# Optimization experiments

Hardware: AMD Instinct MI355X
Metric: run time of the kernel (lower is better)

## Reference

```python
import jax, jax.numpy as jnp
import numpy as np

GAMMA = 5.0 / 3.0
N, H = 131072, 256


def mlp(c, W1, b1, W2, b2, W3, b3, W4, b4):
    h = jnp.tanh(c @ W1 + b1)
    h = jnp.tanh(h @ W2 + b2)
    h = jnp.tanh(h @ W3 + b3)
    return h @ W4 + b4  # [N, 6] -> (rho, vx, vy, Bx, By, P)


def setup_inputs() -> dict:
    key = jax.random.key(0)
    ks = jax.random.split(key, 6)
    s = 0.5
    return {
        "coords": jax.random.uniform(ks[0], (N, 3), jnp.float32),  # (x, y, t)
        "W1": jax.random.normal(ks[1], (3, H), jnp.float32) * s,
        "b1": jnp.zeros((H,), jnp.float32),
        "W2": jax.random.normal(ks[2], (H, H), jnp.float32) * (s / np.sqrt(H)),
        "b2": jnp.zeros((H,), jnp.float32),
        "W3": jax.random.normal(ks[3], (H, H), jnp.float32) * (s / np.sqrt(H)),
        "b3": jnp.zeros((H,), jnp.float32),
        "W4": jax.random.normal(ks[4], (H, 6), jnp.float32) * (s / np.sqrt(H)),
        "b4": jnp.zeros((6,), jnp.float32),
        "weights": jnp.ones((7,), jnp.float32),
    }


def reference(coords, W1, b1, W2, b2, W3, b3, W4, b4, weights):
    f = lambda c: mlp(c, W1, b1, W2, b2, W3, b3, W4, b4)
    preds = f(coords)
    # Batched Jacobian d preds / d coords via 3 forward-mode JVPs (basis dirs x,y,t)
    eye = jnp.eye(3, dtype=coords.dtype)
    jvp1 = lambda e: jax.jvp(f, (coords,), (jnp.broadcast_to(e, coords.shape),))[1]
    J = jnp.transpose(jax.vmap(jvp1)(eye), (1, 2, 0))  # [N, 6, 3]

    rho, vx, vy, Bx, By, P = (preds[:, k] for k in range(6))
    Jx, Jy, Jt = J[..., 0], J[..., 1], J[..., 2]  # each [N, 6]

    # time derivatives (chain rule for composite fields)
    dt_rho = Jt[:, 0]
    dt_Bx, dt_By = Jt[:, 3], Jt[:, 4]
    dt_rhovx = dt_rho * vx + rho * Jt[:, 1]
    dt_rhovy = dt_rho * vy + rho * Jt[:, 2]

    def dE(Jc):  # derivative of total energy E along coord c
        return (Jc[:, 5] / (GAMMA - 1.0)
                + 0.5 * Jc[:, 0] * (vx ** 2 + vy ** 2)
                + rho * (vx * Jc[:, 1] + vy * Jc[:, 2])
                + Bx * Jc[:, 3] + By * Jc[:, 4])

    dE_dx, dE_dy, dE_dt = dE(Jx), dE(Jy), dE(Jt)

    div_v = Jx[:, 1] + Jy[:, 2]
    div_B = Jx[:, 3] + Jy[:, 4]
    continuity = dt_rho + rho * div_v

    # grad of total pressure P + 0.5*(Bx^2 + By^2)
    dPm_dx = Jx[:, 5] + Bx * Jx[:, 3] + By * Jx[:, 4]
    dPm_dy = Jy[:, 5] + Bx * Jy[:, 3] + By * Jy[:, 4]
    momentum_x = dt_rhovx + dPm_dx - (Bx * Jx[:, 3] + By * Jy[:, 3])
    momentum_y = dt_rhovy + dPm_dy - (Bx * Jx[:, 4] + By * Jy[:, 4])

    # induction: G = vx*By - vy*Bx
    def dG(Jc):
        return Jc[:, 1] * By + vx * Jc[:, 4] - Jc[:, 2] * Bx - vy * Jc[:, 3]

    induction_x = dt_Bx + dG(Jy)
    induction_y = dt_By - dG(Jx)

    # energy: d/dt E + div( S*v - D*B ), S = E + P + Pm, D = B.v
    E = P / (GAMMA - 1.0) + 0.5 * rho * (vx ** 2 + vy ** 2) + 0.5 * (Bx ** 2 + By ** 2)
    S = E + P + 0.5 * (Bx ** 2 + By ** 2)
    dS_dx = dE_dx + Jx[:, 5] + Bx * Jx[:, 3] + By * Jx[:, 4]
    dS_dy = dE_dy + Jy[:, 5] + Bx * Jy[:, 3] + By * Jy[:, 4]
    D = Bx * vx + By * vy

    def dD(Jc):
        return Jc[:, 3] * vx + Bx * Jc[:, 1] + Jc[:, 4] * vy + By * Jc[:, 2]

    dFx_dx = dS_dx * vx + S * Jx[:, 1] - dD(Jx) * Bx - D * Jx[:, 3]
    dFy_dy = dS_dy * vy + S * Jy[:, 2] - dD(Jy) * By - D * Jy[:, 4]
    energy = dE_dt + dFx_dx + dFy_dy

    res = [continuity, momentum_x, momentum_y, induction_x, induction_y, energy, div_B]
    loss = sum(w * jnp.mean(r ** 2) for w, r in zip(weights, res))
    return loss
```

## Files before the change

### kernel.cpp

```cpp
#include <hip/hip_runtime.h>
#include <hip/hip_bf16.h>
#include <cstdint>


#define LDW 264
#define TPTS 16
#define GRIDB 256

typedef __attribute__((ext_vector_type(8))) short v8h;
typedef __attribute__((ext_vector_type(4))) float v4f;

__device__ __forceinline__ ushort f2b(float f) {
    uint32_t u = __float_as_uint(f);
    u = (u + 0x7fffu + ((u >> 16) & 1u)) >> 16;
    return (ushort)u;
}
__device__ __forceinline__ uint32_t pk2(float a, float b) {
    union { __hip_bfloat162 h2; uint32_t u; } cv;
    cv.h2 = __float22bfloat162_rn(make_float2(a, b));
    return cv.u;
}
__device__ __forceinline__ float fast_tanh(float x) {
    float e = __expf(2.0f * x);
    return 1.0f - 2.0f * __builtin_amdgcn_rcpf(e + 1.0f);
}

__global__ void prep_weights(const float* __restrict__ W2, const float* __restrict__ W3,
                             const float* __restrict__ W4,
                             ushort* __restrict__ Wt2, ushort* __restrict__ Wt3,
                             ushort* __restrict__ Wt4) {
    int idx = blockIdx.x * 256 + threadIdx.x;
    if (idx < 65536) {
        int k = idx >> 8, n = idx & 255;
        Wt2[n * 256 + k] = f2b(W2[k * 256 + n]);
        Wt3[n * 256 + k] = f2b(W3[k * 256 + n]);
    }
    if (idx < 4096) {
        int n = idx >> 8, k = idx & 255;
        Wt4[n * 256 + k] = (n < 6) ? f2b(W4[k * 6 + n]) : (ushort)0;
    }
}

__device__ __forceinline__ void l1_point(ushort* __restrict__ Xd, const float* __restrict__ csb,
                                         int p, int jj0,
                                         float w0a, float w1a, float w2a, float ba,
                                         float w0b, float w1b, float w2b, float bb_) {
    float x = csb[p * 3], yc = csb[p * 3 + 1], tc = csb[p * 3 + 2];
    float pA = fmaf(x, w0a, fmaf(yc, w1a, fmaf(tc, w2a, ba)));
    float pB = fmaf(x, w0b, fmaf(yc, w1b, fmaf(tc, w2b, bb_)));
    float hA = fast_tanh(pA), hB = fast_tanh(pB);
    float dA = 1.0f - hA * hA, dB = 1.0f - hB * hB;
    *(uint32_t*)(&Xd[p * LDW + jj0])        = pk2(hA, hB);
    *(uint32_t*)(&Xd[(16 + p) * LDW + jj0]) = pk2(dA * w0a, dB * w0b);
    *(uint32_t*)(&Xd[(32 + p) * LDW + jj0]) = pk2(dA * w1a, dB * w1b);
    *(uint32_t*)(&Xd[(48 + p) * LDW + jj0]) = pk2(dA * w2a, dB * w2b);
}

__device__ __forceinline__ void dense_layer(const ushort* __restrict__ src,
                                            ushort* __restrict__ dst,
                                            const v8h (*wf)[8],
                                            const float* __restrict__ biasp,
                                            int wvg, int q, int l15) {
    v4f acc[4][4];
    #pragma unroll
    for (int a = 0; a < 4; a++)
        #pragma unroll
        for (int b = 0; b < 4; b++) {
            v4f z = {0.0f, 0.0f, 0.0f, 0.0f};
            acc[a][b] = z;
        }
    #pragma unroll
    for (int nt = 0; nt < 4; nt++) {
        const ushort* cb = &src[(nt * 16 + l15) * LDW + q * 8];
        v8h B[3];
        B[0] = *(const v8h*)(cb);
        B[1] = *(const v8h*)(cb + 32);
        #pragma unroll
        for (int kk = 0; kk < 8; kk++) {
            if (kk < 6)
                B[(kk + 2) % 3] = *(const v8h*)(cb + (kk + 2) * 32);
            const v8h Bc = B[kk % 3];
            #pragma unroll
            for (int mt = 0; mt < 4; mt++)
                acc[mt][nt] = __builtin_amdgcn_mfma_f32_16x16x32_bf16(
                                  wf[mt][kk], Bc, acc[mt][nt], 0, 0, 0);
        }
    }
    #pragma unroll
    for (int mt = 0; mt < 4; mt++) {
        const int nb = wvg * 64 + mt * 16 + q * 4;
        v4f bb = *(const v4f*)(&biasp[nb]);
        float h0 = fast_tanh(acc[mt][0][0] + bb[0]);
        float h1 = fast_tanh(acc[mt][0][1] + bb[1]);
        float h2 = fast_tanh(acc[mt][0][2] + bb[2]);
        float h3 = fast_tanh(acc[mt][0][3] + bb[3]);
        float d0 = 1.0f - h0 * h0, d1 = 1.0f - h1 * h1;
        float d2 = 1.0f - h2 * h2, d3 = 1.0f - h3 * h3;
        uint2 w;
        w.x = pk2(h0, h1); w.y = pk2(h2, h3);
        *(uint2*)(&dst[l15 * LDW + nb]) = w;
        #pragma unroll
        for (int s = 1; s < 4; s++) {
            w.x = pk2(d0 * acc[mt][s][0], d1 * acc[mt][s][1]);
            w.y = pk2(d2 * acc[mt][s][2], d3 * acc[mt][s][3]);
            *(uint2*)(&dst[(s * 16 + l15) * LDW + nb]) = w;
        }
    }
}

__global__ __launch_bounds__(512, 2)
void mhd_fused(const float* __restrict__ coords,
               const float* __restrict__ W1, const float* __restrict__ b1,
               const float* __restrict__ b2, const float* __restrict__ b3,
               const float* __restrict__ b4,
               const float* __restrict__ wts,
               const ushort* __restrict__ Wt2, const ushort* __restrict__ Wt3,
               const ushort* __restrict__ Wt4,
               float* __restrict__ out, int npts, float inv_n) {
    __shared__ ushort XsA[64 * LDW];
    __shared__ ushort XsB[2][64 * LDW];
    __shared__ ushort XsC[64 * LDW];
    __shared__ ushort W4s[16 * LDW];
    __shared__ float  bias_s[512];
    __shared__ float  cs[2][TPTS * 3];
    __shared__ float  Y4[2][4][TPTS][8];

    const int tid  = threadIdx.x;
    const int lane = tid & 63;
    const int wv   = tid >> 6;
    const int q    = lane >> 4;
    const int l15  = lane & 15;
    const int g3   = wv >> 2;
    const int wvg  = wv & 3;

    for (int idx = tid; idx < 16 * 256; idx += 512)
        W4s[(idx >> 8) * LDW + (idx & 255)] = Wt4[idx];
    bias_s[tid] = (tid < 256) ? b2[tid] : b3[tid - 256];

    const ushort* Wsrc = g3 ? Wt3 : Wt2;
    v8h wf[4][8];
    #pragma unroll
    for (int mt = 0; mt < 4; mt++) {
        const int nrow = (wvg * 64 + mt * 16 + l15) * 256 + q * 8;
        #pragma unroll
        for (int kk = 0; kk < 8; kk++)
            wf[mt][kk] = *(const v8h*)(&Wsrc[nrow + kk * 32]);
    }

    const int jj0 = (tid & 127) * 2, half8 = (tid >> 7) * 8;
    float w0a = 0, w1a = 0, w2a = 0, ba = 0, w0b = 0, w1b = 0, w2b = 0, bb_ = 0;
    if (!g3) {
        w0a = W1[jj0];       w1a = W1[256 + jj0];     w2a = W1[512 + jj0];     ba  = b1[jj0];
        w0b = W1[jj0 + 1];   w1b = W1[256 + jj0 + 1]; w2b = W1[512 + jj0 + 1]; bb_ = b1[jj0 + 1];
    }

    const float b40 = b4[0], b41 = b4[1], b42 = b4[2], b43 = b4[3], b44 = b4[4], b45 = b4[5];
    const float wt0 = wts[0], wt1 = wts[1], wt2_ = wts[2], wt3_ = wts[3],
                wt4_ = wts[4], wt5 = wts[5], wt6 = wts[6];

    const int ntiles = (npts + TPTS - 1) / TPTS;
    const int nt_blk = (ntiles > (int)blockIdx.x)
                         ? (ntiles - (int)blockIdx.x + GRIDB - 1) / GRIDB : 0;
    float vsum = 0.0f;

    if (tid < 96) {
        int b = tid / 48, r = tid % 48;
        if (b < nt_blk) {
            int p = r / 3, c = r % 3;
            int gp = ((int)blockIdx.x + b * GRIDB) * TPTS + p;
            if (gp >= npts) gp = npts - 1;
            cs[b][r] = coords[gp * 3 + c];
        }
    }
    __syncthreads();
    if (!g3 && nt_blk > 0) {
        #pragma unroll
        for (int pp = 0; pp < 8; pp++)
            l1_point(XsA, cs[0], half8 + pp, jj0, w0a, w1a, w2a, ba, w0b, w1b, w2b, bb_);
    }
    __syncthreads();

    for (int i = 0; i <= nt_blk + 1; ++i) {
        if (!g3) {
            if (i < nt_blk)
                dense_layer(XsA, XsB[i & 1], wf, bias_s, wvg, q, l15);
        } else {
            if (i >= 1 && i <= nt_blk)
                dense_layer(XsB[(i + 1) & 1], XsC, wf, bias_s + 256, wvg, q, l15);
        }
        __syncthreads();

        if (!g3) {
            if (i + 1 < nt_blk) {
                const float* csb = cs[(i + 1) & 1];
                #pragma unroll
                for (int pp = 0; pp < 8; pp++)
                    l1_point(XsA, csb, half8 + pp, jj0,
                             w0a, w1a, w2a, ba, w0b, w1b, w2b, bb_);
            }
        } else {
            if (i >= 1 && i <= nt_blk) {
                v4f a4 = {0.0f, 0.0f, 0.0f, 0.0f};
                #pragma unroll
                for (int kk = 0; kk < 8; kk++) {
                    v8h A  = *(const v8h*)(&W4s[l15 * LDW + kk * 32 + q * 8]);
                    v8h Bf = *(const v8h*)(&XsC[(wvg * 16 + l15) * LDW + kk * 32 + q * 8]);
                    a4 = __builtin_amdgcn_mfma_f32_16x16x32_bf16(A, Bf, a4, 0, 0, 0);
                }
                if (q < 2) {
                    #pragma unroll
                    for (int r = 0; r < 4; r++)
                        Y4[(i + 1) & 1][wvg][l15][q * 4 + r] = a4[r];
                }
            }
            if (wv == 4 && lane < 16 && i >= 2) {
                const int pb = ((int)blockIdx.x + (i - 2) * GRIDB) * TPTS;
                if (pb + lane < npts) {
                    const int ib = i & 1;
                    const float* Yh = Y4[ib][0][lane];
                    const float* JX = Y4[ib][1][lane];
                    const float* JY = Y4[ib][2][lane];
                    const float* JT = Y4[ib][3][lane];
                    const float g1 = 1.5f;
                    float rho = Yh[0] + b40, vx = Yh[1] + b41, vy = Yh[2] + b42;
                    float Bx  = Yh[3] + b43, By = Yh[4] + b44, P  = Yh[5] + b45;
                    float v2 = vx * vx + vy * vy;
                    float dt_rho = JT[0];
                    float dt_rhovx = dt_rho * vx + rho * JT[1];
                    float dt_rhovy = dt_rho * vy + rho * JT[2];
                    auto dE = [&](const float* J) {
                        return J[5] * g1 + 0.5f * J[0] * v2 + rho * (vx * J[1] + vy * J[2]) + Bx * J[3] + By * J[4];
                    };
                    float dE_dx = dE(JX), dE_dy = dE(JY), dE_dt = dE(JT);
                    float div_v = JX[1] + JY[2];
                    float div_B = JX[3] + JY[4];
                    float continuity = dt_rho + rho * div_v;
                    float dPm_dx = JX[5] + Bx * JX[3] + By * JX[4];
                    float dPm_dy = JY[5] + Bx * JY[3] + By * JY[4];
                    float momentum_x = dt_rhovx + dPm_dx - (Bx * JX[3] + By * JY[3]);
                    float momentum_y = dt_rhovy + dPm_dy - (Bx * JX[4] + By * JY[4]);
                    auto dG = [&](const float* J) {
                        return J[1] * By + vx * J[4] - J[2] * Bx - vy * J[3];
                    };
                    float induction_x = JT[3] + dG(JY);
                    float induction_y = JT[4] - dG(JX);
                    float E = P * g1 + 0.5f * rho * v2 + 0.5f * (Bx * Bx + By * By);
                    float S = E + P + 0.5f * (Bx * Bx + By * By);
                    float dS_dx = dE_dx + JX[5] + Bx * JX[3] + By * JX[4];
                    float dS_dy = dE_dy + JY[5] + Bx * JY[3] + By * JY[4];
                    float D = Bx * vx + By * vy;
                    auto dD = [&](const float* J) {
                        return J[3] * vx + Bx * J[1] + J[4] * vy + By * J[2];
                    };
                    float dFx_dx = dS_dx * vx + S * JX[1] - dD(JX) * Bx - D * JX[3];
                    float dFy_dy = dS_dy * vy + S * JY[2] - dD(JY) * By - D * JY[4];
                    float energy = dE_dt + dFx_dx + dFy_dy;
                    vsum += wt0 * continuity * continuity
                          + wt1 * momentum_x * momentum_x
                          + wt2_ * momentum_y * momentum_y
                          + wt3_ * induction_x * induction_x
                          + wt4_ * induction_y * induction_y
                          + wt5 * energy * energy
                          + wt6 * div_B * div_B;
                }
            }
            if (wv == 7 && lane < 48 && (i + 2) < nt_blk) {
                int p = lane / 3, c = lane % 3;
                int gp = ((int)blockIdx.x + (i + 2) * GRIDB) * TPTS + p;
                if (gp >= npts) gp = npts - 1;
                cs[i & 1][lane] = coords[gp * 3 + c];
            }
        }
        __syncthreads();
    }

    if (wv == 4) {
        #pragma unroll
        for (int off = 8; off >= 1; off >>= 1)
            vsum += __shfl_down(vsum, off, 64);
        if (lane == 0) atomicAdd(out, vsum * inv_n);
    }
}

extern "C" void kernel_launch(void* const* d_in, const int* in_sizes, int n_in,
                              void* d_out, int out_size, void* d_ws, size_t ws_size,
                              hipStream_t stream) {
    const float* coords = (const float*)d_in[0];
    const float* W1 = (const float*)d_in[1];
    const float* b1 = (const float*)d_in[2];
    const float* W2 = (const float*)d_in[3];
    const float* b2 = (const float*)d_in[4];
    const float* W3 = (const float*)d_in[5];
    const float* b3 = (const float*)d_in[6];
    const float* W4 = (const float*)d_in[7];
    const float* b4 = (const float*)d_in[8];
    const float* wts = (const float*)d_in[9];
    const int npts = in_sizes[0] / 3;

    ushort* Wt2 = (ushort*)d_ws;
    ushort* Wt3 = Wt2 + 65536;
    ushort* Wt4 = Wt3 + 65536;

    hipMemsetAsync(d_out, 0, sizeof(float), stream);
    prep_weights<<<256, 256, 0, stream>>>(W2, W3, W4, Wt2, Wt3, Wt4);
    mhd_fused<<<GRIDB, 512, 0, stream>>>(coords, W1, b1, b2, b3, b4, wts,
                                         Wt2, Wt3, Wt4, (float*)d_out, npts, 1.0f / npts);
}
```

Measured before the change: 221.1 us.

## Double block size to 1024 threads and split each layer's weight rows across more waves

Raises the workgroup from 8 to 16 waves. Each wave of the two dense-layer groups now owns 32 output rows instead of 64, which halves the register-resident weight fragments and accumulators per wave. Layer-1 weights move from registers to shared memory, and the output-layer MFMA, residual and coordinate-prefetch work go to dedicated waves in the second group. The aim is more waves per CU to hide MFMA and LDS latency. The cost is heavier barrier synchronisation, and the (1024,4) launch bound may force a tight register cap that causes spills.

```diff
diff --git a/kernel.cpp b/kernel.cpp
--- a/kernel.cpp
+++ b/kernel.cpp
@@ -61,9 +61,9 @@
                                             const v8h (*wf)[8],
                                             const float* __restrict__ biasp,
                                             int wvg, int q, int l15) {
-    v4f acc[4][4];
+    v4f acc[2][4];
     #pragma unroll
-    for (int a = 0; a < 4; a++)
+    for (int a = 0; a < 2; a++)
         #pragma unroll
         for (int b = 0; b < 4; b++) {
             v4f z = {0.0f, 0.0f, 0.0f, 0.0f};
@@ -81,14 +81,14 @@
                 B[(kk + 2) % 3] = *(const v8h*)(cb + (kk + 2) * 32);
             const v8h Bc = B[kk % 3];
             #pragma unroll
-            for (int mt = 0; mt < 4; mt++)
+            for (int mt = 0; mt < 2; mt++)
                 acc[mt][nt] = __builtin_amdgcn_mfma_f32_16x16x32_bf16(
                                   wf[mt][kk], Bc, acc[mt][nt], 0, 0, 0);
         }
     }
     #pragma unroll
-    for (int mt = 0; mt < 4; mt++) {
-        const int nb = wvg * 64 + mt * 16 + q * 4;
+    for (int mt = 0; mt < 2; mt++) {
+        const int nb = wvg * 32 + mt * 16 + q * 4;
         v4f bb = *(const v4f*)(&biasp[nb]);
         float h0 = fast_tanh(acc[mt][0][0] + bb[0]);
         float h1 = fast_tanh(acc[mt][0][1] + bb[1]);
@@ -108,7 +108,7 @@
     }
 }
 
-__global__ __launch_bounds__(512, 2)
+__global__ __launch_bounds__(1024, 4)
 void mhd_fused(const float* __restrict__ coords,
                const float* __restrict__ W1, const float* __restrict__ b1,
                const float* __restrict__ b2, const float* __restrict__ b3,
@@ -122,6 +122,7 @@
     __shared__ ushort XsC[64 * LDW];
     __shared__ ushort W4s[16 * LDW];
     __shared__ float  bias_s[512];
+    __shared__ float  l1w_s[256 * 4];
     __shared__ float  cs[2][TPTS * 3];
     __shared__ float  Y4[2][4][TPTS][8];
 
@@ -130,28 +131,27 @@
     const int wv   = tid >> 6;
     const int q    = lane >> 4;
     const int l15  = lane & 15;
-    const int g3   = wv >> 2;
-    const int wvg  = wv & 3;
-
-    for (int idx = tid; idx < 16 * 256; idx += 512)
+    const int g3   = wv >> 3;
+    const int wvg  = wv & 7;
+
+    for (int idx = tid; idx < 16 * 256; idx += 1024)
         W4s[(idx >> 8) * LDW + (idx & 255)] = Wt4[idx];
-    bias_s[tid] = (tid < 256) ? b2[tid] : b3[tid - 256];
+    if (tid < 512) bias_s[tid] = (tid < 256) ? b2[tid] : b3[tid - 256];
+    if (tid < 256) {
+        l1w_s[tid * 4 + 0] = W1[tid];
+        l1w_s[tid * 4 + 1] = W1[256 + tid];
+        l1w_s[tid * 4 + 2] = W1[512 + tid];
+        l1w_s[tid * 4 + 3] = b1[tid];
+    }
 
     const ushort* Wsrc = g3 ? Wt3 : Wt2;
-    v8h wf[4][8];
+    v8h wf[2][8];
     #pragma unroll
-    for (int mt = 0; mt < 4; mt++) {
-        const int nrow = (wvg * 64 + mt * 16 + l15) * 256 + q * 8;
+    for (int mt = 0; mt < 2; mt++) {
+        const int nrow = (wvg * 32 + mt * 16 + l15) * 256 + q * 8;
         #pragma unroll
         for (int kk = 0; kk < 8; kk++)
             wf[mt][kk] = *(const v8h*)(&Wsrc[nrow + kk * 32]);
-    }
-
-    const int jj0 = (tid & 127) * 2, half8 = (tid >> 7) * 8;
-    float w0a = 0, w1a = 0, w2a = 0, ba = 0, w0b = 0, w1b = 0, w2b = 0, bb_ = 0;
-    if (!g3) {
-        w0a = W1[jj0];       w1a = W1[256 + jj0];     w2a = W1[512 + jj0];     ba  = b1[jj0];
-        w0b = W1[jj0 + 1];   w1b = W1[256 + jj0 + 1]; w2b = W1[512 + jj0 + 1]; bb_ = b1[jj0 + 1];
     }
 
     const float b40 = b4[0], b41 = b4[1], b42 = b4[2], b43 = b4[3], b44 = b4[4], b45 = b4[5];
@@ -162,6 +162,8 @@
     const int nt_blk = (ntiles > (int)blockIdx.x)
                          ? (ntiles - (int)blockIdx.x + GRIDB - 1) / GRIDB : 0;
     float vsum = 0.0f;
+
+    const int jj0 = (tid & 127) * 2, half8 = ((tid >> 7) & 1) * 8;
 
     if (tid < 96) {
         int b = tid / 48, r = tid % 48;
@@ -173,10 +175,13 @@
         }
     }
     __syncthreads();
-    if (!g3 && nt_blk > 0) {
+    if (tid < 256 && nt_blk > 0) {
+        const v4f ca = *(const v4f*)(&l1w_s[jj0 * 4]);
+        const v4f cb2 = *(const v4f*)(&l1w_s[jj0 * 4 + 4]);
         #pragma unroll
         for (int pp = 0; pp < 8; pp++)
-            l1_point(XsA, cs[0], half8 + pp, jj0, w0a, w1a, w2a, ba, w0b, w1b, w2b, bb_);
+            l1_point(XsA, cs[0], half8 + pp, jj0,
+                     ca[0], ca[1], ca[2], ca[3], cb2[0], cb2[1], cb2[2], cb2[3]);
     }
     __syncthreads();
 
@@ -190,30 +195,34 @@
         }
         __syncthreads();
 
-        if (!g3) {
+        if (tid < 256) {
             if (i + 1 < nt_blk) {
                 const float* csb = cs[(i + 1) & 1];
+                const v4f ca = *(const v4f*)(&l1w_s[jj0 * 4]);
+                const v4f cb2 = *(const v4f*)(&l1w_s[jj0 * 4 + 4]);
                 #pragma unroll
                 for (int pp = 0; pp < 8; pp++)
                     l1_point(XsA, csb, half8 + pp, jj0,
-                             w0a, w1a, w2a, ba, w0b, w1b, w2b, bb_);
+                             ca[0], ca[1], ca[2], ca[3], cb2[0], cb2[1], cb2[2], cb2[3]);
             }
-        } else {
+        } else if (wv >= 8 && wv < 12) {
             if (i >= 1 && i <= nt_blk) {
+                const int sv = wv & 3;
                 v4f a4 = {0.0f, 0.0f, 0.0f, 0.0f};
                 #pragma unroll
                 for (int kk = 0; kk < 8; kk++) {
                     v8h A  = *(const v8h*)(&W4s[l15 * LDW + kk * 32 + q * 8]);
-                    v8h Bf = *(const v8h*)(&XsC[(wvg * 16 + l15) * LDW + kk * 32 + q * 8]);
+                    v8h Bf = *(const v8h*)(&XsC[(sv * 16 + l15) * LDW + kk * 32 + q * 8]);
                     a4 = __builtin_amdgcn_mfma_f32_16x16x32_bf16(A, Bf, a4, 0, 0, 0);
                 }
                 if (q < 2) {
                     #pragma unroll
                     for (int r = 0; r < 4; r++)
-                        Y4[(i + 1) & 1][wvg][l15][q * 4 + r] = a4[r];
+                        Y4[(i + 1) & 1][sv][l15][q * 4 + r] = a4[r];
                 }
             }
-            if (wv == 4 && lane < 16 && i >= 2) {
+        } else if (wv == 12) {
+            if (lane < 16 && i >= 2) {
                 const int pb = ((int)blockIdx.x + (i - 2) * GRIDB) * TPTS;
                 if (pb + lane < npts) {
                     const int ib = i & 1;
@@ -264,7 +273,8 @@
                           + wt6 * div_B * div_B;
                 }
             }
-            if (wv == 7 && lane < 48 && (i + 2) < nt_blk) {
+        } else if (wv == 15) {
+            if (lane < 48 && (i + 2) < nt_blk) {
                 int p = lane / 3, c = lane % 3;
                 int gp = ((int)blockIdx.x + (i + 2) * GRIDB) * TPTS + p;
                 if (gp >= npts) gp = npts - 1;
@@ -274,7 +284,7 @@
         __syncthreads();
     }
 
-    if (wv == 4) {
+    if (wv == 12) {
         #pragma unroll
         for (int off = 8; off >= 1; off >>= 1)
             vsum += __shfl_down(vsum, off, 64);
@@ -303,6 +313,6 @@
 
     hipMemsetAsync(d_out, 0, sizeof(float), stream);
     prep_weights<<<256, 256, 0, stream>>>(W2, W3, W4, Wt2, Wt3, Wt4);
-    mhd_fused<<<GRIDB, 512, 0, stream>>>(coords, W1, b1, b2, b3, b4, wts,
-                                         Wt2, Wt3, Wt4, (float*)d_out, npts, 1.0f / npts);
-}
+    mhd_fused<<<GRIDB, 1024, 0, stream>>>(coords, W1, b1, b2, b3, b4, wts,
+                                          Wt2, Wt3, Wt4, (float*)d_out, npts, 1.0f / npts);
+}
```

Result: slower. 252.6 us (+14.3%).
